# Kernel tuning notes

Measured on AMD Instinct MI355X. Metric: run time of the kernel, lower is better.

The kernel has to match this reference:

```python
import jax, jax.numpy as jnp
import numpy as np


def setup_inputs() -> dict:
    key = jax.random.key(0)
    k1, k2, k3, k4 = jax.random.split(key, 4)
    T, D, N = 8192, 128, 32
    x = jax.random.normal(k1, (T, D), dtype=jnp.float32)
    h_a0 = jax.random.normal(k2, (N, D), dtype=jnp.float32)
    h_sd0 = jax.random.uniform(k3, (N, D), dtype=jnp.float32)
    alpha = jax.random.uniform(k4, (N, D), dtype=jnp.float32)  # nn.Parameter uniform(0,1)
    return {"x": x, "h_a0": h_a0, "h_sd0": h_sd0, "alpha": alpha}


def reference(x, h_a0, h_sd0, alpha):
    # EMA with standard deviation (with_SD=True), expressed as a lax.scan
    # over the time axis. h state: (h_a, h_v) each (num_N, input_dim).
    h_v0 = h_sd0 ** 2

    def step(carry, x_i):
        h_a, h_v = carry
        d = x_i[None, :] - h_a            # (N, D)
        h_v = (1.0 - alpha) * (h_v + alpha * d * d)
        h_a = h_a + alpha * d
        return (h_a, h_v), (h_a, h_v)

    (hN_a, hN_v), (out_a, out_v) = jax.lax.scan(step, (h_a0, h_v0), x)
    # out_a/out_v: (T, N, D); torch code concatenates avg and sqrt(var) on dim 1
    out = jnp.concatenate([out_a, jnp.sqrt(out_v)], axis=1)  # (T, 2N, D)
    return out, hN_a, jnp.sqrt(hN_v)
```

## Files before the change

### kernel.cpp

```cpp
#include <hip/hip_runtime.h>
#include <math.h>

typedef float vf4 __attribute__((ext_vector_type(4)));

constexpr int T = 8192;
constexpr int D = 128;
constexpr int N = 32;
constexpr int L = 32;
constexpr int LOG2L = 5;
constexpr int K = T / L;
constexpr int S = N * D;
constexpr int S4 = S / 4;
constexpr int D4 = D / 4;
constexpr int OSTRIDE4 = (2 * N * D) / 4;

constexpr int SEG  = 8;
constexpr int CPS  = K / SEG;
constexpr int COLS = 32;

__device__ __forceinline__ float fast_sqrt(float x) {
    float r;
    asm("v_sqrt_f32 %0, %1" : "=v"(r) : "v"(x));
    return r;
}

__global__ __launch_bounds__(256) void k1_summaries(
    const vf4* __restrict__ x, const vf4* __restrict__ alpha,
    vf4* __restrict__ c_a, vf4* __restrict__ cA, vf4* __restrict__ cP)
{
    int gid = blockIdx.x * 256 + threadIdx.x;
    int k   = gid >> 10;
    int s4  = gid & (S4 - 1);
    int d4  = s4 & (D4 - 1);

    vf4 a = alpha[s4];
    vf4 b = 1.0f - a;
    vf4 q = {0.f, 0.f, 0.f, 0.f};
    vf4 A = {0.f, 0.f, 0.f, 0.f};
    vf4 P = {0.f, 0.f, 0.f, 0.f};
    const vf4* xp = x + (size_t)k * L * D4 + d4;
#pragma unroll 8
    for (int i = 0; i < L; ++i) {
        vf4 xv = xp[(size_t)i * D4];
        vf4 p  = xv - q;
        P += p;
        A = b * (A + (a * p) * p);
        q = q + a * p;
    }
    c_a[gid] = q;
    cA[gid]  = A;
    cP[gid]  = P;
}

__global__ __launch_bounds__(256) void k2_scan(
    const vf4* __restrict__ h_a0, const vf4* __restrict__ h_sd0,
    const vf4* __restrict__ alpha,
    vf4* __restrict__ buf0,
    vf4* __restrict__ buf1,
    const vf4* __restrict__ buf2,
    float* __restrict__ out)
{
    __shared__ vf4 Cagg[SEG][COLS];
    __shared__ vf4 Vagg[SEG][COLS];

    int t   = threadIdx.x;
    int col = t & (COLS - 1);
    int kg  = t >> 5;
    int s4  = blockIdx.x * COLS + col;
    int kbase = kg * CPS;

    vf4 a = alpha[s4];
    vf4 b = 1.0f - a;
    vf4 bl = b;
#pragma unroll
    for (int i = 0; i < LOG2L; ++i) bl *= bl;
    vf4 M = bl;
#pragma unroll
    for (int i = 0; i < 5; ++i) M *= M;
    vf4 Cq = bl * (1.0f - bl);
    vf4 Bc = a * bl;

    vf4 C = {0.f, 0.f, 0.f, 0.f};
#pragma unroll 4
    for (int j = 0; j < CPS; ++j) {
        vf4 ca = buf0[(size_t)(kbase + j) * S4 + s4];
        C = bl * C + ca;
    }
    Cagg[kg][col] = C;
    __syncthreads();

    vf4 H = h_a0[s4];
    for (int g = 0; g < kg; ++g) H = M * H + Cagg[g][col];

    vf4 Vg = {0.f, 0.f, 0.f, 0.f};
#pragma unroll 4
    for (int j = 0; j < CPS; ++j) {
        size_t idx = (size_t)(kbase + j) * S4 + s4;
        vf4 ca = buf0[idx];
        vf4 Ak = buf1[idx];
        vf4 Pk = buf2[idx];
        buf0[idx] = H;
        vf4 cv = Ak - 2.0f * ((Bc * Pk) * H) + Cq * (H * H);
        Vg = bl * Vg + cv;
        H  = bl * H + ca;
    }
    Vagg[kg][col] = Vg;
    if (kg == SEG - 1) {
        vf4* tail = (vf4*)(out + (size_t)T * 2 * N * D);
        tail[s4] = H;
    }
    __syncthreads();

    vf4 sd = h_sd0[s4];
    vf4 V = sd * sd;
    for (int g = 0; g < kg; ++g) V = M * V + Vagg[g][col];

#pragma unroll 4
    for (int j = 0; j < CPS; ++j) {
        size_t idx = (size_t)(kbase + j) * S4 + s4;
        vf4 Hk = buf0[idx];
        vf4 Ak = buf1[idx];
        vf4 Pk = buf2[idx];
        vf4 Vc;
#pragma unroll
        for (int jj = 0; jj < 4; ++jj) Vc[jj] = fmaxf(V[jj], 0.f);
        buf1[idx] = Vc;
        vf4 cv = Ak - 2.0f * ((Bc * Pk) * Hk) + Cq * (Hk * Hk);
        V = bl * Vc + cv;
    }
    if (kg == SEG - 1) {
        vf4* tail = (vf4*)(out + (size_t)T * 2 * N * D);
        vf4 r;
#pragma unroll
        for (int jj = 0; jj < 4; ++jj) r[jj] = fast_sqrt(fmaxf(V[jj], 0.f));
        tail[S4 + s4] = r;
    }
}

__global__ __launch_bounds__(256) void k3_fused(
    const vf4* __restrict__ x, const vf4* __restrict__ alpha,
    const vf4* __restrict__ h_a_start, const vf4* __restrict__ h_v_start,
    vf4* __restrict__ out)
{
    int gid = blockIdx.x * 256 + threadIdx.x;
    int k   = gid >> 10;
    int s4  = gid & (S4 - 1);
    int n   = s4 >> 5;
    int d4  = s4 & (D4 - 1);

    vf4 a = alpha[s4];
    vf4 b = 1.0f - a;
    vf4 h = h_a_start[gid];
    vf4 v = h_v_start[gid];
    const vf4* xp = x + (size_t)k * L * D4 + d4;
    vf4* opa = out + (size_t)k * L * OSTRIDE4 + n * D4 + d4;
    vf4* opv = opa + N * D4;
#pragma unroll 8
    for (int i = 0; i < L; ++i) {
        vf4 xv  = xp[(size_t)i * D4];
        vf4 dx  = xv - h;
        vf4 adx = a * dx;
        v = b * (v + adx * dx);
        h = h + adx;
        vf4 r;
#pragma unroll
        for (int j = 0; j < 4; ++j) r[j] = fast_sqrt(v[j]);
        __builtin_nontemporal_store(h, &opa[(size_t)i * OSTRIDE4]);
        __builtin_nontemporal_store(r, &opv[(size_t)i * OSTRIDE4]);
    }
}

extern "C" void kernel_launch(void* const* d_in, const int* in_sizes, int n_in,
                              void* d_out, int out_size, void* d_ws, size_t ws_size,
                              hipStream_t stream) {
    const vf4* x     = (const vf4*)d_in[0];
    const vf4* h_a0  = (const vf4*)d_in[1];
    const vf4* h_sd0 = (const vf4*)d_in[2];
    const vf4* alpha = (const vf4*)d_in[3];
    float* out = (float*)d_out;
    float* ws  = (float*)d_ws;

    vf4* buf0 = (vf4*)(ws + 0 * (size_t)K * S);
    vf4* buf1 = (vf4*)(ws + 1 * (size_t)K * S);
    vf4* buf2 = (vf4*)(ws + 2 * (size_t)K * S);

    dim3 big(K * S4 / 256);
    dim3 blk(256);

    k1_summaries<<<big, blk, 0, stream>>>(x, alpha, buf0, buf1, buf2);
    k2_scan<<<dim3(S4 / COLS), blk, 0, stream>>>(h_a0, h_sd0, alpha,
                                                 buf0, buf1, buf2, out);
    k3_fused<<<big, blk, 0, stream>>>(x, alpha, buf0, buf1, (vf4*)out);
}
```

Before: 293.5 us.

## Restructure output kernel to one block per chunk with four states per thread

The final output kernel now launches one block per time chunk, and each thread handles four (n,d4) states that share the same x column. Each x load is reused four times instead of once, and every output row of 2N*D floats is written by one block as fully contiguous stores. Non-temporal stores are dropped in favour of plain stores. The grid shrinks fourfold (256 blocks), and each thread carries more registers and less parallelism, which could hurt latency hiding on the write-bound output path.

```diff
diff --git a/kernel.cpp b/kernel.cpp
--- a/kernel.cpp
+++ b/kernel.cpp
@@ -16,6 +16,7 @@
 
 constexpr int SEG  = 8;
 constexpr int CPS  = K / SEG;
+constexpr int LOG2CPS = 5;
 constexpr int COLS = 32;
 
 __device__ __forceinline__ float fast_sqrt(float x) {
@@ -76,16 +77,14 @@
     for (int i = 0; i < LOG2L; ++i) bl *= bl;
     vf4 M = bl;
 #pragma unroll
-    for (int i = 0; i < 5; ++i) M *= M;
+    for (int i = 0; i < LOG2CPS; ++i) M *= M;
     vf4 Cq = bl * (1.0f - bl);
     vf4 Bc = a * bl;
 
     vf4 C = {0.f, 0.f, 0.f, 0.f};
 #pragma unroll 4
-    for (int j = 0; j < CPS; ++j) {
-        vf4 ca = buf0[(size_t)(kbase + j) * S4 + s4];
-        C = bl * C + ca;
-    }
+    for (int j = 0; j < CPS; ++j)
+        C = bl * C + buf0[(size_t)(kbase + j) * S4 + s4];
     Cagg[kg][col] = C;
     __syncthreads();
 
@@ -106,13 +105,12 @@
     }
     Vagg[kg][col] = Vg;
     if (kg == SEG - 1) {
-        vf4* tail = (vf4*)(out + (size_t)T * 2 * N * D);
-        tail[s4] = H;
+        ((vf4*)(out + (size_t)T * 2 * N * D))[s4] = H;
     }
     __syncthreads();
 
-    vf4 sd = h_sd0[s4];
-    vf4 V = sd * sd;
+    vf4 sdv = h_sd0[s4];
+    vf4 V = sdv * sdv;
     for (int g = 0; g < kg; ++g) V = M * V + Vagg[g][col];
 
 #pragma unroll 4
@@ -129,44 +127,50 @@
         V = bl * Vc + cv;
     }
     if (kg == SEG - 1) {
-        vf4* tail = (vf4*)(out + (size_t)T * 2 * N * D);
         vf4 r;
 #pragma unroll
         for (int jj = 0; jj < 4; ++jj) r[jj] = fast_sqrt(fmaxf(V[jj], 0.f));
-        tail[S4 + s4] = r;
+        ((vf4*)(out + (size_t)T * 2 * N * D))[S4 + s4] = r;
     }
 }
 
-__global__ __launch_bounds__(256) void k3_fused(
+__global__ __launch_bounds__(256) void k3_rows(
     const vf4* __restrict__ x, const vf4* __restrict__ alpha,
     const vf4* __restrict__ h_a_start, const vf4* __restrict__ h_v_start,
     vf4* __restrict__ out)
 {
-    int gid = blockIdx.x * 256 + threadIdx.x;
-    int k   = gid >> 10;
-    int s4  = gid & (S4 - 1);
-    int n   = s4 >> 5;
-    int d4  = s4 & (D4 - 1);
+    const int k   = blockIdx.x;
+    const int tid = threadIdx.x;
+    const int d4  = tid & (D4 - 1);
 
-    vf4 a = alpha[s4];
-    vf4 b = 1.0f - a;
-    vf4 h = h_a_start[gid];
-    vf4 v = h_v_start[gid];
-    const vf4* xp = x + (size_t)k * L * D4 + d4;
-    vf4* opa = out + (size_t)k * L * OSTRIDE4 + n * D4 + d4;
-    vf4* opv = opa + N * D4;
-#pragma unroll 8
+    vf4 a[4], b[4], h[4], v[4];
+#pragma unroll
+    for (int j = 0; j < 4; ++j) {
+        int s4 = tid + 256 * j;
+        a[j] = alpha[s4];
+        b[j] = 1.0f - a[j];
+        h[j] = h_a_start[(size_t)k * S4 + s4];
+        v[j] = h_v_start[(size_t)k * S4 + s4];
+    }
+
+    const vf4* xp   = x + (size_t)k * L * D4 + d4;
+    vf4*       orow = out + (size_t)k * L * OSTRIDE4;
+
     for (int i = 0; i < L; ++i) {
-        vf4 xv  = xp[(size_t)i * D4];
-        vf4 dx  = xv - h;
-        vf4 adx = a * dx;
-        v = b * (v + adx * dx);
-        h = h + adx;
-        vf4 r;
+        vf4 xv = xp[(size_t)i * D4];
 #pragma unroll
-        for (int j = 0; j < 4; ++j) r[j] = fast_sqrt(v[j]);
-        __builtin_nontemporal_store(h, &opa[(size_t)i * OSTRIDE4]);
-        __builtin_nontemporal_store(r, &opv[(size_t)i * OSTRIDE4]);
+        for (int j = 0; j < 4; ++j) {
+            vf4 dx  = xv - h[j];
+            vf4 adx = a[j] * dx;
+            v[j] = b[j] * (v[j] + adx * dx);
+            h[j] = h[j] + adx;
+            vf4 r;
+#pragma unroll
+            for (int jj = 0; jj < 4; ++jj) r[jj] = fast_sqrt(v[j][jj]);
+            orow[tid + 256 * j]        = h[j];
+            orow[1024 + tid + 256 * j] = r;
+        }
+        orow += OSTRIDE4;
     }
 }
 
@@ -184,11 +188,10 @@
     vf4* buf1 = (vf4*)(ws + 1 * (size_t)K * S);
     vf4* buf2 = (vf4*)(ws + 2 * (size_t)K * S);
 
-    dim3 big(K * S4 / 256);
     dim3 blk(256);
 
-    k1_summaries<<<big, blk, 0, stream>>>(x, alpha, buf0, buf1, buf2);
+    k1_summaries<<<dim3(K * S4 / 256), blk, 0, stream>>>(x, alpha, buf0, buf1, buf2);
     k2_scan<<<dim3(S4 / COLS), blk, 0, stream>>>(h_a0, h_sd0, alpha,
                                                  buf0, buf1, buf2, out);
-    k3_fused<<<big, blk, 0, stream>>>(x, alpha, buf0, buf1, (vf4*)out);
+    k3_rows<<<dim3(K), blk, 0, stream>>>(x, alpha, buf0, buf1, (vf4*)out);
 }
```

Result: no change. 298.2 us (+1.6%).
